# Optimization experiments

Measured on AMD Instinct MI355X. Metric: run time of the kernel, lower is better.

Reference implementation:

```python
import jax, jax.numpy as jnp
import numpy as np

B, IN_DIM, OUT_DIM, NUM_FN = 256, 65536, 65536, 16  # fan_in=2 -> 16 logic functions


def setup_inputs() -> dict:
    key = jax.random.key(0)
    k1, k2, k3 = jax.random.split(key, 3)
    x = jax.random.uniform(k1, (B, IN_DIM), dtype=jnp.float32)
    weights = jax.random.normal(k2, (OUT_DIM, NUM_FN), dtype=jnp.float32)
    # each output neuron picks fan_in=2 input wires
    indices = jax.random.randint(k3, (2, OUT_DIM), 0, IN_DIM, dtype=jnp.int64)
    return {"x": x, "weights": weights, "indices": indices}


def _logic_ops(a, b):
    """All 16 real-valued relaxations of binary boolean functions. [B,OUT,16]."""
    ab = a * b
    one = jnp.ones_like(a)
    zero = jnp.zeros_like(a)
    return jnp.stack([
        zero,                # 0: false
        ab,                  # 1: a AND b
        a - ab,              # 2: a AND NOT b
        a,                   # 3: a
        b - ab,              # 4: NOT a AND b
        b,                   # 5: b
        a + b - 2 * ab,      # 6: a XOR b
        a + b - ab,          # 7: a OR b
        1 - (a + b - ab),    # 8: NOR
        1 - (a + b - 2*ab),  # 9: XNOR
        1 - b,               # 10: NOT b
        1 - b + ab,          # 11: a OR NOT b
        1 - a,               # 12: NOT a
        1 - a + ab,          # 13: NOT a OR b
        1 - ab,              # 14: NAND
        one,                 # 15: true
    ], axis=-1)


def reference(x, weights, indices):
    # gather fan-in inputs: a, b each [B, OUT_DIM]
    a = x[..., indices[0]]
    b = x[..., indices[1]]
    probs = jax.nn.softmax(weights, axis=-1)        # [OUT_DIM, 16] (training path)
    ops = _logic_ops(a, b)                          # [B, OUT_DIM, 16]
    return jnp.einsum('bof,of->bo', ops, probs)     # softmax-weighted combo
```

## Files before the change

kernel.cpp:

```cpp
#include <hip/hip_runtime.h>

#define IN_DIM  65536
#define OUT_DIM 65536
#define BATCH   256


__device__ __forceinline__ float bf2f(unsigned short h) {
    return __uint_as_float(((unsigned int)h) << 16);
}
__device__ __forceinline__ unsigned short f2bf(float f) {
    unsigned int u = __float_as_uint(f);
    u += 0x7FFFu + ((u >> 16) & 1u);
    return (unsigned short)(u >> 16);
}

__device__ __forceinline__ float4 collapse16(const float* w) {
    float m = w[0];
    #pragma unroll
    for (int f = 1; f < 16; ++f) m = fmaxf(m, w[f]);
    float e[16]; float sum = 0.f;
    #pragma unroll
    for (int f = 0; f < 16; ++f) { e[f] = __expf(w[f] - m); sum += e[f]; }
    float inv = 1.0f / sum;
    float w0 = e[8] + e[9] + e[10] + e[11] + e[12] + e[13] + e[14] + e[15];
    float w1 = (e[2] + e[3] + e[6] + e[7]) - (e[8] + e[9] + e[12] + e[13]);
    float w2 = (e[4] + e[5] + e[6] + e[7]) - (e[8] + e[9] + e[10] + e[11]);
    float w3 = e[1] - e[2] - e[4] - 2.f*e[6] - e[7]
             + e[8] + 2.f*e[9] + e[11] + e[13] - e[14];
    return make_float4(w0 * inv, w1 * inv, w2 * inv, w3 * inv);
}

#define TRANS_BLOCKS ((IN_DIM / 64) * (BATCH / 64))
#define COEFF_BLOCKS (OUT_DIM / 256)

__global__ __launch_bounds__(256) void prep_kernel(
    const void* __restrict__ x_raw,
    const void* __restrict__ w_raw,
    unsigned int* __restrict__ x_Tb,
    float4* __restrict__ coeffs,
    int trans_blocks)
{
    __shared__ float tile[64][65];
    __shared__ int sflag;
    int t  = threadIdx.x;
    int bx = blockIdx.x;

    if (bx < trans_blocks) {
        if (t == 0) sflag = 0;
        __syncthreads();
        if (((const unsigned short*)x_raw)[t] >= 0x3F80u) atomicOr(&sflag, 1);
        __syncthreads();
        int x_is_f32 = sflag;

        int c0 = (bx >> 2) * 64;
        int b0 = (bx & 3) * 64;
        int tx = t & 63, ty = t >> 6;

        if (x_is_f32) {
            const float* x = (const float*)x_raw;
            #pragma unroll
            for (int k = 0; k < 64; k += 4)
                tile[ty + k][tx] = x[(size_t)(b0 + ty + k) * IN_DIM + c0 + tx];
        } else {
            const unsigned short* x = (const unsigned short*)x_raw;
            #pragma unroll
            for (int k = 0; k < 64; k += 4)
                tile[ty + k][tx] = bf2f(x[(size_t)(b0 + ty + k) * IN_DIM + c0 + tx]);
        }
        __syncthreads();
        #pragma unroll
        for (int k = 0; k < 8; ++k) {
            int d   = t + 256 * k;
            int col = d >> 5;
            int dw  = d & 31;
            float lo = tile[2 * dw][col];
            float hi = tile[2 * dw + 1][col];
            unsigned int p = (unsigned int)f2bf(lo) | ((unsigned int)f2bf(hi) << 16);
            x_Tb[(size_t)(c0 + col) * (BATCH / 2) + (b0 >> 1) + dw] = p;
        }
    } else {
        if (t == 0) sflag = 0;
        __syncthreads();
        if ((((const unsigned short*)w_raw)[t] & 0x7FFFu) >= 0x4800u) atomicOr(&sflag, 1);
        __syncthreads();
        int w_is_f32 = sflag;

        int o = (bx - trans_blocks) * 256 + t;
        if (o >= OUT_DIM) return;

        float w[16];
        if (w_is_f32) {
            const float4* w4 = reinterpret_cast<const float4*>(w_raw) + (size_t)o * 4;
            float4 q0 = w4[0], q1 = w4[1], q2 = w4[2], q3 = w4[3];
            w[0]=q0.x; w[1]=q0.y; w[2]=q0.z; w[3]=q0.w;
            w[4]=q1.x; w[5]=q1.y; w[6]=q1.z; w[7]=q1.w;
            w[8]=q2.x; w[9]=q2.y; w[10]=q2.z; w[11]=q2.w;
            w[12]=q3.x; w[13]=q3.y; w[14]=q3.z; w[15]=q3.w;
        } else {
            const uint4* w16 = reinterpret_cast<const uint4*>(
                (const unsigned short*)w_raw + (size_t)o * 16);
            uint4 p0 = w16[0], p1 = w16[1];
            unsigned int pk[8] = { p0.x, p0.y, p0.z, p0.w, p1.x, p1.y, p1.z, p1.w };
            #pragma unroll
            for (int i = 0; i < 8; ++i) {
                w[2*i]   = bf2f((unsigned short)(pk[i] & 0xFFFFu));
                w[2*i+1] = bf2f((unsigned short)(pk[i] >> 16));
            }
        }
        coeffs[o] = collapse16(w);
    }
}

#define ROWS_PER_CHUNK 32

__global__ __launch_bounds__(256) void logic_bt_kernel(
    const unsigned int* __restrict__ x_Tb,
    const void* __restrict__ idx_raw,
    const float4* __restrict__ coeffs,
    float* __restrict__ out)
{
    __shared__ int sflag;
    int t = threadIdx.x;
    if (t == 0) sflag = 0;
    __syncthreads();
    if ((t & 1) && ((const int*)idx_raw)[t] != 0) atomicOr(&sflag, 1);
    __syncthreads();
    int idx_is_i32 = sflag;

    int o = blockIdx.x * 256 + t;
    int ia, ib;
    if (idx_is_i32) {
        const int* p = (const int*)idx_raw;
        ia = p[o];       ib = p[OUT_DIM + o];
    } else {
        const long long* p = (const long long*)idx_raw;
        ia = (int)p[o];  ib = (int)p[OUT_DIM + o];
    }
    float4 c = coeffs[o];

    int b0 = blockIdx.y * ROWS_PER_CHUNK;
    const uint4* xa = (const uint4*)x_Tb + ((size_t)ia << 5) + (b0 >> 3);
    const uint4* xb = (const uint4*)x_Tb + ((size_t)ib << 5) + (b0 >> 3);

    #pragma unroll
    for (int r = 0; r < ROWS_PER_CHUNK / 8; ++r) {
        uint4 ua = xa[r], ub = xb[r];
        unsigned int pa[4] = { ua.x, ua.y, ua.z, ua.w };
        unsigned int pb[4] = { ub.x, ub.y, ub.z, ub.w };
        int base = b0 + r * 8;
        #pragma unroll
        for (int j = 0; j < 4; ++j) {
            float a0 = bf2f((unsigned short)(pa[j] & 0xFFFFu));
            float a1 = bf2f((unsigned short)(pa[j] >> 16));
            float v0 = bf2f((unsigned short)(pb[j] & 0xFFFFu));
            float v1 = bf2f((unsigned short)(pb[j] >> 16));
            float r0 = fmaf(v0, fmaf(c.w, a0, c.z), fmaf(c.y, a0, c.x));
            float r1 = fmaf(v1, fmaf(c.w, a1, c.z), fmaf(c.y, a1, c.x));
            out[(size_t)(base + 2*j)     * OUT_DIM + o] = r0;
            out[(size_t)(base + 2*j + 1) * OUT_DIM + o] = r1;
        }
    }
}

__global__ __launch_bounds__(256) void logic_direct_kernel(
    const void* __restrict__ x_raw,
    const void* __restrict__ idx_raw,
    const float4* __restrict__ coeffs,
    float* __restrict__ out)
{
    __shared__ int sflag;
    int t = threadIdx.x;
    if (t == 0) sflag = 0;
    __syncthreads();
    int fl = 0;
    if (((const unsigned short*)x_raw)[t] >= 0x3F80u) fl |= 1;
    if ((t & 1) && ((const int*)idx_raw)[t] != 0) fl |= 2;
    if (fl) atomicOr(&sflag, fl);
    __syncthreads();
    int x_is_f32   = sflag & 1;
    int idx_is_i32 = (sflag >> 1) & 1;

    int o = blockIdx.x * 256 + t;
    int ia, ib;
    if (idx_is_i32) {
        const int* p = (const int*)idx_raw;
        ia = p[o];       ib = p[OUT_DIM + o];
    } else {
        const long long* p = (const long long*)idx_raw;
        ia = (int)p[o];  ib = (int)p[OUT_DIM + o];
    }
    float4 c = coeffs[o];
    int b0 = blockIdx.y * ROWS_PER_CHUNK;

    if (x_is_f32) {
        const float* xa = (const float*)x_raw + ia;
        const float* xb = (const float*)x_raw + ib;
        #pragma unroll 8
        for (int r = 0; r < ROWS_PER_CHUNK; ++r) {
            int b = b0 + r;
            float av = xa[(size_t)b * IN_DIM];
            float bv = xb[(size_t)b * IN_DIM];
            out[(size_t)b * OUT_DIM + o] =
                fmaf(bv, fmaf(c.w, av, c.z), fmaf(c.y, av, c.x));
        }
    } else {
        const unsigned short* xa = (const unsigned short*)x_raw + ia;
        const unsigned short* xb = (const unsigned short*)x_raw + ib;
        #pragma unroll 8
        for (int r = 0; r < ROWS_PER_CHUNK; ++r) {
            int b = b0 + r;
            float av = bf2f(xa[(size_t)b * IN_DIM]);
            float bv = bf2f(xb[(size_t)b * IN_DIM]);
            out[(size_t)b * OUT_DIM + o] =
                fmaf(bv, fmaf(c.w, av, c.z), fmaf(c.y, av, c.x));
        }
    }
}

extern "C" void kernel_launch(void* const* d_in, const int* in_sizes, int n_in,
                              void* d_out, int out_size, void* d_ws, size_t ws_size,
                              hipStream_t stream) {
    const void* x       = d_in[0];
    const void* weights = d_in[1];
    const void* indices = d_in[2];
    float*      out     = (float*)d_out;

    float4*       coeffs = (float4*)((char*)d_ws + 256);
    unsigned int* x_Tb   = (unsigned int*)((char*)d_ws + 2u * 1024u * 1024u);

    const size_t need = 2u * 1024u * 1024u +
                        (size_t)IN_DIM * (BATCH / 2) * sizeof(unsigned int);

    if (ws_size >= need) {
        prep_kernel<<<dim3(TRANS_BLOCKS + COEFF_BLOCKS), dim3(256), 0, stream>>>(
            x, weights, x_Tb, coeffs, TRANS_BLOCKS);
        dim3 grid(OUT_DIM / 256, BATCH / ROWS_PER_CHUNK);
        logic_bt_kernel<<<grid, dim3(256), 0, stream>>>(
            x_Tb, indices, coeffs, out);
    } else {
        prep_kernel<<<dim3(COEFF_BLOCKS), dim3(256), 0, stream>>>(
            x, weights, x_Tb, coeffs, 0);
        dim3 grid(OUT_DIM / 256, BATCH / ROWS_PER_CHUNK);
        logic_direct_kernel<<<grid, dim3(256), 0, stream>>>(
            x, indices, coeffs, out);
    }
}
```

Baseline: 140.2 us.

## Vectorize transpose loads/stores and process two outputs per thread in gather kernel

The transpose prep now reads x with float4 (or packed bf16 pairs), pads the shared tile to 69 columns, and writes the packed bf16 transposed rows as uint4 stores. The main gather kernel handles two adjacent outputs per thread, issuing all 16 uint4 gather loads up front and writing float2 output stores, with half as many blocks along the output dimension. The aim is fewer, wider memory transactions and more loads in flight per thread. In exchange it uses more registers per thread and there are fewer threads in the grid to hide latency.

After: 142.4 us. No clear change (+1.5%).

```diff
diff --git a/kernel.cpp b/kernel.cpp
--- a/kernel.cpp
+++ b/kernel.cpp
@@ -32,6 +32,7 @@
 
 #define TRANS_BLOCKS ((IN_DIM / 64) * (BATCH / 64))
 #define COEFF_BLOCKS (OUT_DIM / 256)
+#define PAD 69
 
 __global__ __launch_bounds__(256) void prep_kernel(
     const void* __restrict__ x_raw,
@@ -40,7 +41,7 @@
     float4* __restrict__ coeffs,
     int trans_blocks)
 {
-    __shared__ float tile[64][65];
+    __shared__ float tile[64][PAD];
     __shared__ int sflag;
     int t  = threadIdx.x;
     int bx = blockIdx.x;
@@ -54,29 +55,49 @@
 
         int c0 = (bx >> 2) * 64;
         int b0 = (bx & 3) * 64;
-        int tx = t & 63, ty = t >> 6;
+        int cq = t & 15;
+        int r  = t >> 4;
 
         if (x_is_f32) {
-            const float* x = (const float*)x_raw;
-            #pragma unroll
-            for (int k = 0; k < 64; k += 4)
-                tile[ty + k][tx] = x[(size_t)(b0 + ty + k) * IN_DIM + c0 + tx];
+            const float4* x4 = (const float4*)x_raw;
+            #pragma unroll
+            for (int k = 0; k < 4; ++k) {
+                int row = r + 16 * k;
+                float4 v = x4[(size_t)(b0 + row) * (IN_DIM / 4) + (c0 >> 2) + cq];
+                tile[row][4 * cq + 0] = v.x;
+                tile[row][4 * cq + 1] = v.y;
+                tile[row][4 * cq + 2] = v.z;
+                tile[row][4 * cq + 3] = v.w;
+            }
         } else {
-            const unsigned short* x = (const unsigned short*)x_raw;
-            #pragma unroll
-            for (int k = 0; k < 64; k += 4)
-                tile[ty + k][tx] = bf2f(x[(size_t)(b0 + ty + k) * IN_DIM + c0 + tx]);
-        }
-        __syncthreads();
+            const uint2* x2 = (const uint2*)x_raw;
+            #pragma unroll
+            for (int k = 0; k < 4; ++k) {
+                int row = r + 16 * k;
+                uint2 v = x2[(size_t)(b0 + row) * (IN_DIM / 4) + (c0 >> 2) + cq];
+                tile[row][4 * cq + 0] = bf2f((unsigned short)(v.x & 0xFFFFu));
+                tile[row][4 * cq + 1] = bf2f((unsigned short)(v.x >> 16));
+                tile[row][4 * cq + 2] = bf2f((unsigned short)(v.y & 0xFFFFu));
+                tile[row][4 * cq + 3] = bf2f((unsigned short)(v.y >> 16));
+            }
+        }
+        __syncthreads();
+
+        uint4* dst = (uint4*)x_Tb;
+        int q   = t & 7;
+        int col = t >> 3;
         #pragma unroll
-        for (int k = 0; k < 8; ++k) {
-            int d   = t + 256 * k;
-            int col = d >> 5;
-            int dw  = d & 31;
-            float lo = tile[2 * dw][col];
-            float hi = tile[2 * dw + 1][col];
-            unsigned int p = (unsigned int)f2bf(lo) | ((unsigned int)f2bf(hi) << 16);
-            x_Tb[(size_t)(c0 + col) * (BATCH / 2) + (b0 >> 1) + dw] = p;
+        for (int it = 0; it < 2; ++it) {
+            int cc = col + 32 * it;
+            unsigned int d[4];
+            #pragma unroll
+            for (int j = 0; j < 4; ++j) {
+                float lo = tile[8 * q + 2 * j][cc];
+                float hi = tile[8 * q + 2 * j + 1][cc];
+                d[j] = (unsigned int)f2bf(lo) | ((unsigned int)f2bf(hi) << 16);
+            }
+            dst[(size_t)(c0 + cc) * (BATCH / 8) + (b0 >> 3) + q] =
+                make_uint4(d[0], d[1], d[2], d[3]);
         }
     } else {
         if (t == 0) sflag = 0;
@@ -111,8 +132,6 @@
     }
 }
 
-#define ROWS_PER_CHUNK 32
-
 __global__ __launch_bounds__(256) void logic_bt_kernel(
     const unsigned int* __restrict__ x_Tb,
     const void* __restrict__ idx_raw,
@@ -127,37 +146,63 @@
     __syncthreads();
     int idx_is_i32 = sflag;
 
-    int o = blockIdx.x * 256 + t;
-    int ia, ib;
+    int o0 = blockIdx.x * 512 + 2 * t;
+    int o1 = o0 + 1;
+    int ia0, ib0, ia1, ib1;
     if (idx_is_i32) {
         const int* p = (const int*)idx_raw;
-        ia = p[o];       ib = p[OUT_DIM + o];
+        ia0 = p[o0];           ia1 = p[o1];
+        ib0 = p[OUT_DIM + o0]; ib1 = p[OUT_DIM + o1];
     } else {
         const long long* p = (const long long*)idx_raw;
-        ia = (int)p[o];  ib = (int)p[OUT_DIM + o];
-    }
-    float4 c = coeffs[o];
-
-    int b0 = blockIdx.y * ROWS_PER_CHUNK;
-    const uint4* xa = (const uint4*)x_Tb + ((size_t)ia << 5) + (b0 >> 3);
-    const uint4* xb = (const uint4*)x_Tb + ((size_t)ib << 5) + (b0 >> 3);
-
-    #pragma unroll
-    for (int r = 0; r < ROWS_PER_CHUNK / 8; ++r) {
-        uint4 ua = xa[r], ub = xb[r];
-        unsigned int pa[4] = { ua.x, ua.y, ua.z, ua.w };
-        unsigned int pb[4] = { ub.x, ub.y, ub.z, ub.w };
+        ia0 = (int)p[o0];           ia1 = (int)p[o1];
+        ib0 = (int)p[OUT_DIM + o0]; ib1 = (int)p[OUT_DIM + o1];
+    }
+    float4 c0 = coeffs[o0];
+    float4 c1 = coeffs[o1];
+
+    int b0 = blockIdx.y * 32;
+    int qo = b0 >> 3;
+    const uint4* A0 = (const uint4*)x_Tb + ((size_t)ia0 << 5) + qo;
+    const uint4* B0 = (const uint4*)x_Tb + ((size_t)ib0 << 5) + qo;
+    const uint4* A1 = (const uint4*)x_Tb + ((size_t)ia1 << 5) + qo;
+    const uint4* B1 = (const uint4*)x_Tb + ((size_t)ib1 << 5) + qo;
+
+    uint4 a0[4], v0[4], a1[4], v1[4];
+    #pragma unroll
+    for (int r = 0; r < 4; ++r) {
+        a0[r] = A0[r]; v0[r] = B0[r];
+        a1[r] = A1[r]; v1[r] = B1[r];
+    }
+
+    float2* out2 = (float2*)(out + o0);
+
+    #pragma unroll
+    for (int r = 0; r < 4; ++r) {
+        unsigned int pa0[4] = { a0[r].x, a0[r].y, a0[r].z, a0[r].w };
+        unsigned int pb0[4] = { v0[r].x, v0[r].y, v0[r].z, v0[r].w };
+        unsigned int pa1[4] = { a1[r].x, a1[r].y, a1[r].z, a1[r].w };
+        unsigned int pb1[4] = { v1[r].x, v1[r].y, v1[r].z, v1[r].w };
         int base = b0 + r * 8;
         #pragma unroll
         for (int j = 0; j < 4; ++j) {
-            float a0 = bf2f((unsigned short)(pa[j] & 0xFFFFu));
-            float a1 = bf2f((unsigned short)(pa[j] >> 16));
-            float v0 = bf2f((unsigned short)(pb[j] & 0xFFFFu));
-            float v1 = bf2f((unsigned short)(pb[j] >> 16));
-            float r0 = fmaf(v0, fmaf(c.w, a0, c.z), fmaf(c.y, a0, c.x));
-            float r1 = fmaf(v1, fmaf(c.w, a1, c.z), fmaf(c.y, a1, c.x));
-            out[(size_t)(base + 2*j)     * OUT_DIM + o] = r0;
-            out[(size_t)(base + 2*j + 1) * OUT_DIM + o] = r1;
+            float xa0 = bf2f((unsigned short)(pa0[j] & 0xFFFFu));
+            float ya0 = bf2f((unsigned short)(pa0[j] >> 16));
+            float xb0 = bf2f((unsigned short)(pb0[j] & 0xFFFFu));
+            float yb0 = bf2f((unsigned short)(pb0[j] >> 16));
+            float xa1 = bf2f((unsigned short)(pa1[j] & 0xFFFFu));
+            float ya1 = bf2f((unsigned short)(pa1[j] >> 16));
+            float xb1 = bf2f((unsigned short)(pb1[j] & 0xFFFFu));
+            float yb1 = bf2f((unsigned short)(pb1[j] >> 16));
+
+            float2 r0, r1;
+            r0.x = fmaf(xb0, fmaf(c0.w, xa0, c0.z), fmaf(c0.y, xa0, c0.x));
+            r0.y = fmaf(xb1, fmaf(c1.w, xa1, c1.z), fmaf(c1.y, xa1, c1.x));
+            r1.x = fmaf(yb0, fmaf(c0.w, ya0, c0.z), fmaf(c0.y, ya0, c0.x));
+            r1.y = fmaf(yb1, fmaf(c1.w, ya1, c1.z), fmaf(c1.y, ya1, c1.x));
+
+            out2[(size_t)(base + 2 * j)     * (OUT_DIM / 2)] = r0;
+            out2[(size_t)(base + 2 * j + 1) * (OUT_DIM / 2)] = r1;
         }
     }
 }
@@ -190,13 +235,13 @@
         ia = (int)p[o];  ib = (int)p[OUT_DIM + o];
     }
     float4 c = coeffs[o];
-    int b0 = blockIdx.y * ROWS_PER_CHUNK;
+    int b0 = blockIdx.y * 32;
 
     if (x_is_f32) {
         const float* xa = (const float*)x_raw + ia;
         const float* xb = (const float*)x_raw + ib;
         #pragma unroll 8
-        for (int r = 0; r < ROWS_PER_CHUNK; ++r) {
+        for (int r = 0; r < 32; ++r) {
             int b = b0 + r;
             float av = xa[(size_t)b * IN_DIM];
             float bv = xb[(size_t)b * IN_DIM];
@@ -207,7 +252,7 @@
         const unsigned short* xa = (const unsigned short*)x_raw + ia;
         const unsigned short* xb = (const unsigned short*)x_raw + ib;
         #pragma unroll 8
-        for (int r = 0; r < ROWS_PER_CHUNK; ++r) {
+        for (int r = 0; r < 32; ++r) {
             int b = b0 + r;
             float av = bf2f(xa[(size_t)b * IN_DIM]);
             float bv = bf2f(xb[(size_t)b * IN_DIM]);
@@ -234,13 +279,13 @@
     if (ws_size >= need) {
         prep_kernel<<<dim3(TRANS_BLOCKS + COEFF_BLOCKS), dim3(256), 0, stream>>>(
             x, weights, x_Tb, coeffs, TRANS_BLOCKS);
-        dim3 grid(OUT_DIM / 256, BATCH / ROWS_PER_CHUNK);
+        dim3 grid(OUT_DIM / 512, BATCH / 32);
         logic_bt_kernel<<<grid, dim3(256), 0, stream>>>(
             x_Tb, indices, coeffs, out);
     } else {
         prep_kernel<<<dim3(COEFF_BLOCKS), dim3(256), 0, stream>>>(
             x, weights, x_Tb, coeffs, 0);
-        dim3 grid(OUT_DIM / 256, BATCH / ROWS_PER_CHUNK);
+        dim3 grid(OUT_DIM / 256, BATCH / 32);
         logic_direct_kernel<<<grid, dim3(256), 0, stream>>>(
             x, indices, coeffs, out);
     }
```
